# Performance work log

Hardware: AMD Instinct MI355X
Metric: run time of the kernel (lower is better)

The kernel has to match this reference:

```python
import jax, jax.numpy as jnp
import numpy as np


def gru_cell(x, h, Wi, Wh, bi, bh):
    # PyTorch GRU gate order: r, z, n
    gi = x @ Wi + bi
    gh = h @ Wh + bh
    ir, iz, inn = jnp.split(gi, 3, axis=-1)
    hr, hz, hn = jnp.split(gh, 3, axis=-1)
    r = jax.nn.sigmoid(ir + hr)
    z = jax.nn.sigmoid(iz + hz)
    n = jnp.tanh(inn + r * hn)
    return (1.0 - z) * n + z * h


def run_gru_dir(emb, lens, Wi, Wh, bi, bh, reverse):
    # Masked GRU emulating pack_padded_sequence: state holds once t >= len,
    # padded output positions are zero (as pad_packed_sequence produces).
    B, S, _ = emb.shape
    H = Wh.shape[0]
    xs = jnp.swapaxes(emb, 0, 1)  # [S, B, E]
    ts = jnp.arange(S)
    if reverse:
        xs = xs[::-1]
        ts = ts[::-1]
    def step(h, inp):
        x, t = inp
        valid = (t < lens)[:, None]
        h_new = jnp.where(valid, gru_cell(x, h, Wi, Wh, bi, bh), h)
        return h_new, jnp.where(valid, h_new, 0.0)
    hT, outs = jax.lax.scan(step, jnp.zeros((B, H), emb.dtype), (xs, ts))
    if reverse:
        outs = outs[::-1]
    return jnp.swapaxes(outs, 0, 1), hT  # [B,S,H], [B,H]


def seq2seq_forward(src, trg, src_lens, enc_embed, Wi_f, Wh_f, bi_f, bh_f,
                    Wi_b, Wh_b, bi_b, bh_b, W_e2d, b_e2d, dec_embed,
                    Wi_d, Wh_d, bi_d, bh_d, Wq, bq, Wk, bk, Wv, bv,
                    W1, b1, W2, b2):
    lens = jnp.clip(src_lens, 1, None)
    emb = enc_embed[src]  # [B,S,E]; dropout is identity in eval
    out_f, h_f = run_gru_dir(emb, lens, Wi_f, Wh_f, bi_f, bh_f, False)
    out_b, h_b = run_gru_dir(emb, lens, Wi_b, Wh_b, bi_b, bh_b, True)
    word_reps = jnp.concatenate([out_f, out_b], axis=-1)  # [B,S,2H]
    sent_rep = jnp.concatenate([h_f, h_b], axis=-1)       # [B,2H]
    hidden0 = jax.nn.gelu(sent_rep @ W_e2d + b_e2d, approximate=False)
    # k/v projections are loop-invariant -> hoist (same math as per-step)
    K = word_reps @ Wk + bk   # [B,S,kq]
    V = word_reps @ Wv + bv   # [B,S,D]
    scale = 1.0 / np.sqrt(Wq.shape[1]).astype(np.float32)
    def dec_step(h_prev, tok):
        e = dec_embed[tok]  # [B,E]
        h = gru_cell(e, h_prev, Wi_d, Wh_d, bi_d, bh_d)
        q = h @ Wq + bq
        alpha = jax.nn.softmax(jnp.einsum('bk,bsk->bs', q, K) * scale, axis=-1)
        attn = jnp.einsum('bs,bsd->bd', alpha, V)
        hid = h + attn
        out = jax.nn.gelu(hid @ W1 + b1, approximate=False) @ W2 + b2
        return hid, out
    toks = trg[:, :-1].T  # [T-1, B]
    _, outs = jax.lax.scan(dec_step, hidden0, toks)  # [T-1, B, V]
    B = trg.shape[0]
    V = W2.shape[1]
    # outputs[:, 0, :] stays zero as in the original preallocated buffer
    return jnp.concatenate(
        [jnp.zeros((B, 1, V), outs.dtype), jnp.swapaxes(outs, 0, 1)], axis=1)


def setup_inputs() -> dict:
    key = jax.random.key(0)
    ks = iter(jax.random.split(key, 32))
    B, S, T = 32, 64, 64
    SV, TV, E, H, D, KQ = 32000, 32000, 256, 512, 512, 64
    def nrm(shape, fan_in):
        return jax.random.normal(next(ks), shape, jnp.float32) / np.sqrt(fan_in).astype(np.float32)
    return {
        'src': jax.random.randint(next(ks), (B, S), 0, SV),
        'trg': jax.random.randint(next(ks), (B, T), 0, TV),
        'src_lens': jax.random.randint(next(ks), (B,), 1, S + 1),
        'enc_embed': jax.random.normal(next(ks), (SV, E), jnp.float32) * 0.1,
        'Wi_f': nrm((E, 3 * H), E), 'Wh_f': nrm((H, 3 * H), H),
        'bi_f': jnp.zeros((3 * H,), jnp.float32), 'bh_f': jnp.zeros((3 * H,), jnp.float32),
        'Wi_b': nrm((E, 3 * H), E), 'Wh_b': nrm((H, 3 * H), H),
        'bi_b': jnp.zeros((3 * H,), jnp.float32), 'bh_b': jnp.zeros((3 * H,), jnp.float32),
        'W_e2d': nrm((2 * H, D), 2 * H), 'b_e2d': jnp.zeros((D,), jnp.float32),
        'dec_embed': jax.random.normal(next(ks), (TV, E), jnp.float32) * 0.1,
        'Wi_d': nrm((E, 3 * D), E), 'Wh_d': nrm((D, 3 * D), D),
        'bi_d': jnp.zeros((3 * D,), jnp.float32), 'bh_d': jnp.zeros((3 * D,), jnp.float32),
        'Wq': nrm((D, KQ), D), 'bq': jnp.zeros((KQ,), jnp.float32),
        'Wk': nrm((2 * H, KQ), 2 * H), 'bk': jnp.zeros((KQ,), jnp.float32),
        'Wv': nrm((2 * H, D), 2 * H), 'bv': jnp.zeros((D,), jnp.float32),
        'W1': nrm((D, D), D), 'b1': jnp.zeros((D,), jnp.float32),
        'W2': nrm((D, TV), D), 'b2': jnp.zeros((TV,), jnp.float32),
    }


def reference(src, trg, src_lens, enc_embed, Wi_f, Wh_f, bi_f, bh_f,
              Wi_b, Wh_b, bi_b, bh_b, W_e2d, b_e2d, dec_embed,
              Wi_d, Wh_d, bi_d, bh_d, Wq, bq, Wk, bk, Wv, bv,
              W1, b1, W2, b2):
    return seq2seq_forward(src, trg, src_lens, enc_embed, Wi_f, Wh_f, bi_f, bh_f,
                           Wi_b, Wh_b, bi_b, bh_b, W_e2d, b_e2d, dec_embed,
                           Wi_d, Wh_d, bi_d, bh_d, Wq, bq, Wk, bk, Wv, bv,
                           W1, b1, W2, b2)
```

## Files before the change

kernel.cpp:

```cpp
#include <hip/hip_runtime.h>
#include <stdint.h>

typedef unsigned short u16;
typedef short v8s __attribute__((ext_vector_type(8)));
typedef float v4f __attribute__((ext_vector_type(4)));

#define DI static __device__ __forceinline__

DI u16 f2bf(float x){ union{float f; uint32_t u;} c; c.f = x; uint32_t r = c.u + 0x7fffu + ((c.u >> 16) & 1u); return (u16)(r >> 16); }
DI float bf2f(u16 b){ union{float f; uint32_t u;} c; c.u = ((uint32_t)b) << 16; return c.f; }
DI float gelu_f(float x){ return 0.5f * x * (1.0f + erff(x * 0.70710678118654752f)); }
DI float sigm(float x){ return 1.0f / (1.0f + expf(-x)); }

__global__ __launch_bounds__(256) void transpose_split_kernel(
    const float* __restrict__ W, u16* __restrict__ hi, u16* __restrict__ lo, int K, int N)
{
    __shared__ float t[32][33];
    int n0 = blockIdx.x * 32, k0 = blockIdx.y * 32;
    int tx = threadIdx.x & 31, ty = threadIdx.x >> 5;
    #pragma unroll
    for (int i = 0; i < 4; i++) {
        int k = k0 + ty + i * 8, n = n0 + tx;
        float v = (k < K && n < N) ? W[(size_t)k * N + n] : 0.f;
        t[ty + i * 8][tx] = v;
    }
    __syncthreads();
    #pragma unroll
    for (int i = 0; i < 4; i++) {
        int n = n0 + ty + i * 8, k = k0 + tx;
        if (n < N && k < K) {
            float v = t[tx][ty + i * 8];
            u16 h = f2bf(v);
            hi[(size_t)n * K + k] = h;
            lo[(size_t)n * K + k] = f2bf(v - bf2f(h));
        }
    }
}

__global__ __launch_bounds__(256) void gather_init_kernel(
    const int* __restrict__ src, const int* __restrict__ trg,
    const float* __restrict__ enc_embed, const float* __restrict__ dec_embed,
    float* __restrict__ embE, float* __restrict__ embD,
    float* __restrict__ hF0, float* __restrict__ hB0)
{
    int r = blockIdx.x, tx = threadIdx.x;
    if (r < 2048) {
        int idx = src[r];
        embE[(size_t)r * 256 + tx] = enc_embed[(size_t)idx * 256 + tx];
    } else if (r < 4064) {
        int rd = r - 2048;
        int t = rd >> 5, b = rd & 31;
        int tok = trg[b * 64 + t];
        embD[(size_t)rd * 256 + tx] = dec_embed[(size_t)tok * 256 + tx];
    } else {
        int i = (r - 4064) * 256 + tx;
        if (i < 16384) hF0[i] = 0.f; else hB0[i - 16384] = 0.f;
    }
}

__global__ __launch_bounds__(256) void gemm_bf16x3_kernel(
    const float* __restrict__ A, const u16* __restrict__ Bhi, const u16* __restrict__ Blo,
    const float* __restrict__ bias, float* __restrict__ C,
    int M, int N, int K, int act_gelu, int remap)
{
    __shared__ u16 Ah[128 * 40], Al[128 * 40], Bh[128 * 40], Bl[128 * 40];
    const int tid = threadIdx.x;
    const int lane = tid & 63, wave = tid >> 6;
    const int lm = lane & 15, quad = lane >> 4;
    const int wm = wave >> 1, wn = wave & 1;
    const int m0 = blockIdx.y * 128, n0 = blockIdx.x * 128;
    const int sr = tid >> 1;
    const int sh = (tid & 1) * 16;

    v4f acc[4][4];
    #pragma unroll
    for (int i = 0; i < 4; i++)
        #pragma unroll
        for (int j = 0; j < 4; j++)
            #pragma unroll
            for (int r = 0; r < 4; r++) acc[i][j][r] = 0.f;

    for (int k0 = 0; k0 < K; k0 += 32) {
        {
            float v[16];
            const int gm = m0 + sr;
            if (gm < M) {
                const float4* p = (const float4*)(A + (size_t)gm * K + k0 + sh);
                #pragma unroll
                for (int i = 0; i < 4; i++) {
                    float4 q = p[i];
                    v[4*i] = q.x; v[4*i+1] = q.y; v[4*i+2] = q.z; v[4*i+3] = q.w;
                }
            } else {
                #pragma unroll
                for (int i = 0; i < 16; i++) v[i] = 0.f;
            }
            v8s h0, h1, l0, l1;
            #pragma unroll
            for (int i = 0; i < 8; i++) {
                u16 ha = f2bf(v[i]);     u16 la = f2bf(v[i] - bf2f(ha));
                u16 hb = f2bf(v[8+i]);   u16 lb = f2bf(v[8+i] - bf2f(hb));
                h0[i] = (short)ha; l0[i] = (short)la; h1[i] = (short)hb; l1[i] = (short)lb;
            }
            *(v8s*)&Ah[sr * 40 + sh] = h0; *(v8s*)&Ah[sr * 40 + sh + 8] = h1;
            *(v8s*)&Al[sr * 40 + sh] = l0; *(v8s*)&Al[sr * 40 + sh + 8] = l1;
        }
        {
            const int gn = n0 + sr;
            v8s b0, b1, c0, c1;
            if (gn < N) {
                const v8s* ph = (const v8s*)(Bhi + (size_t)gn * K + k0 + sh);
                const v8s* pl = (const v8s*)(Blo + (size_t)gn * K + k0 + sh);
                b0 = ph[0]; b1 = ph[1]; c0 = pl[0]; c1 = pl[1];
            } else {
                #pragma unroll
                for (int i = 0; i < 8; i++) { b0[i] = 0; b1[i] = 0; c0[i] = 0; c1[i] = 0; }
            }
            *(v8s*)&Bh[sr * 40 + sh] = b0; *(v8s*)&Bh[sr * 40 + sh + 8] = b1;
            *(v8s*)&Bl[sr * 40 + sh] = c0; *(v8s*)&Bl[sr * 40 + sh + 8] = c1;
        }
        __syncthreads();
        v8s ah[4], al[4], bh[4], bl[4];
        #pragma unroll
        for (int mt = 0; mt < 4; mt++) {
            int off = (wm * 64 + mt * 16 + lm) * 40 + quad * 8;
            ah[mt] = *(v8s*)&Ah[off]; al[mt] = *(v8s*)&Al[off];
        }
        #pragma unroll
        for (int nt = 0; nt < 4; nt++) {
            int off = (wn * 64 + nt * 16 + lm) * 40 + quad * 8;
            bh[nt] = *(v8s*)&Bh[off]; bl[nt] = *(v8s*)&Bl[off];
        }
        #pragma unroll
        for (int mt = 0; mt < 4; mt++)
            #pragma unroll
            for (int nt = 0; nt < 4; nt++) {
                v4f a = acc[mt][nt];
                a = __builtin_amdgcn_mfma_f32_16x16x32_bf16(ah[mt], bh[nt], a, 0, 0, 0);
                a = __builtin_amdgcn_mfma_f32_16x16x32_bf16(ah[mt], bl[nt], a, 0, 0, 0);
                a = __builtin_amdgcn_mfma_f32_16x16x32_bf16(al[mt], bh[nt], a, 0, 0, 0);
                acc[mt][nt] = a;
            }
        __syncthreads();
    }
    #pragma unroll
    for (int nt = 0; nt < 4; nt++) {
        int col = n0 + wn * 64 + nt * 16 + lm;
        if (col >= N) continue;
        float bv = bias ? bias[col] : 0.f;
        #pragma unroll
        for (int mt = 0; mt < 4; mt++) {
            int rbase = m0 + wm * 64 + mt * 16 + quad * 4;
            #pragma unroll
            for (int r = 0; r < 4; r++) {
                int row = rbase + r;
                if (row < M) {
                    float v = acc[mt][nt][r] + bv;
                    if (act_gelu) v = gelu_f(v);
                    size_t drow = remap ? (size_t)((row & 31) * 64 + (row >> 5) + 1) : (size_t)row;
                    C[drow * (size_t)N + col] = v;
                }
            }
        }
    }
}

DI float gru_out(float i0, float i1, float i2, float g0, float g1, float g2,
                 float b0, float b1, float b2, float hprev)
{
    float r = sigm(i0 + g0 + b0);
    float z = sigm(i1 + g1 + b1);
    float n = tanhf(i2 + r * (g2 + b2));
    return (1.f - z) * n + z * hprev;
}

__global__ __launch_bounds__(256) void enc_step_kernel(
    int step,
    const float* __restrict__ hFin, float* __restrict__ hFout,
    const float* __restrict__ hBin, float* __restrict__ hBout,
    const float* __restrict__ giF, const float* __restrict__ giB,
    const float* __restrict__ Wh_f, const float* __restrict__ Wh_b,
    const float* __restrict__ bh_f, const float* __restrict__ bh_b,
    const int* __restrict__ src_lens,
    float* __restrict__ wrep, float* __restrict__ sent)
{
    const int dir = blockIdx.x >> 6;
    const int jb = (blockIdx.x & 63) * 8;
    const int tid = threadIdx.x;
    const int b = tid >> 3, jj = tid & 7, j = jb + jj;
    const float* hin = dir ? hBin : hFin;
    const float* gi  = dir ? giB : giF;
    const float* Wh  = dir ? Wh_b : Wh_f;
    const float* bh  = dir ? bh_b : bh_f;
    float* hout = dir ? hBout : hFout;
    const int t_eff = dir ? (63 - step) : step;

    __shared__ float hl[32 * 132];
    float g0 = 0.f, g1 = 0.f, g2 = 0.f;
    for (int kt = 0; kt < 512; kt += 128) {
        __syncthreads();
        #pragma unroll
        for (int w = 0; w < 4; w++) {
            int flat = (tid + w * 256) * 4;
            int bb = flat >> 7, kk = flat & 127;
            float4 fv = *(const float4*)(hin + bb * 512 + kt + kk);
            *(float4*)&hl[bb * 132 + kk] = fv;
        }
        __syncthreads();
        const float* w0base = Wh + (size_t)kt * 1536 + j;
        #pragma unroll 2
        for (int kk = 0; kk < 128; kk += 4) {
            float4 hv = *(const float4*)&hl[b * 132 + kk];
            const float* w = w0base + (size_t)kk * 1536;
            g0 += hv.x * w[0];    g1 += hv.x * w[512];  g2 += hv.x * w[1024];
            g0 += hv.y * w[1536]; g1 += hv.y * w[2048]; g2 += hv.y * w[2560];
            g0 += hv.z * w[3072]; g1 += hv.z * w[3584]; g2 += hv.z * w[4096];
            g0 += hv.w * w[4608]; g1 += hv.w * w[5120]; g2 += hv.w * w[5632];
        }
    }
    size_t gbase = ((size_t)b * 64 + t_eff) * 1536 + j;
    float hprev = hin[b * 512 + j];
    float hnew = gru_out(gi[gbase], gi[gbase + 512], gi[gbase + 1024],
                         g0, g1, g2, bh[j], bh[512 + j], bh[1024 + j], hprev);
    int len = src_lens[b]; if (len < 1) len = 1;
    bool valid = t_eff < len;
    float hkeep = valid ? hnew : hprev;
    hout[b * 512 + j] = hkeep;
    wrep[((size_t)b * 64 + t_eff) * 1024 + dir * 512 + j] = valid ? hnew : 0.f;
    if (step == 63) sent[b * 1024 + dir * 512 + j] = hkeep;
}

__global__ __launch_bounds__(256) void dec_cell_kernel(
    int t, const float* __restrict__ HID, const float* __restrict__ giD,
    const float* __restrict__ Wh, const float* __restrict__ bh,
    float* __restrict__ htmp)
{
    const int jb = blockIdx.x * 8;
    const int tid = threadIdx.x;
    const int b = tid >> 3, jj = tid & 7, j = jb + jj;
    const float* hin = HID + (size_t)t * 16384;

    __shared__ float hl[32 * 132];
    float g0 = 0.f, g1 = 0.f, g2 = 0.f;
    for (int kt = 0; kt < 512; kt += 128) {
        __syncthreads();
        #pragma unroll
        for (int w = 0; w < 4; w++) {
            int flat = (tid + w * 256) * 4;
            int bb = flat >> 7, kk = flat & 127;
            float4 fv = *(const float4*)(hin + bb * 512 + kt + kk);
            *(float4*)&hl[bb * 132 + kk] = fv;
        }
        __syncthreads();
        const float* w0base = Wh + (size_t)kt * 1536 + j;
        #pragma unroll 2
        for (int kk = 0; kk < 128; kk += 4) {
            float4 hv = *(const float4*)&hl[b * 132 + kk];
            const float* w = w0base + (size_t)kk * 1536;
            g0 += hv.x * w[0];    g1 += hv.x * w[512];  g2 += hv.x * w[1024];
            g0 += hv.y * w[1536]; g1 += hv.y * w[2048]; g2 += hv.y * w[2560];
            g0 += hv.z * w[3072]; g1 += hv.z * w[3584]; g2 += hv.z * w[4096];
            g0 += hv.w * w[4608]; g1 += hv.w * w[5120]; g2 += hv.w * w[5632];
        }
    }
    size_t gbase = ((size_t)t * 32 + b) * 1536 + j;
    float hprev = hin[b * 512 + j];
    float hnew = gru_out(giD[gbase], giD[gbase + 512], giD[gbase + 1024],
                         g0, g1, g2, bh[j], bh[512 + j], bh[1024 + j], hprev);
    htmp[b * 512 + j] = hnew;
}

__global__ __launch_bounds__(256) void dec_attn_kernel(
    int t, const float* __restrict__ htmp, const float* __restrict__ Kmat,
    const float* __restrict__ Vmat, const float* __restrict__ Wq,
    const float* __restrict__ bq, float* __restrict__ HID)
{
    const int b = blockIdx.x, tid = threadIdx.x;
    __shared__ float hl[512];
    __shared__ float Kt[64 * 68];
    __shared__ float qp[256];
    __shared__ float qv[64];
    __shared__ float aw[64];

    hl[tid] = htmp[b * 512 + tid];
    hl[256 + tid] = htmp[b * 512 + 256 + tid];
    #pragma unroll
    for (int w = 0; w < 4; w++) {
        int flat = (tid + w * 256) * 4;
        int s = flat >> 6, d = flat & 63;
        float4 fv = *(const float4*)(Kmat + ((size_t)b * 64 + s) * 64 + d);
        *(float4*)&Kt[s * 68 + d] = fv;
    }
    __syncthreads();
    {
        int o = tid >> 2, part = tid & 3;
        float acc = 0.f;
        const float* wq = Wq + (size_t)(part * 128) * 64 + o;
        int base = part * 128;
        for (int k = 0; k < 128; k++) acc += hl[base + k] * wq[(size_t)k * 64];
        qp[tid] = acc;
    }
    __syncthreads();
    if (tid < 64) qv[tid] = qp[tid * 4] + qp[tid * 4 + 1] + qp[tid * 4 + 2] + qp[tid * 4 + 3] + bq[tid];
    __syncthreads();
    if (tid < 64) {
        float sc = 0.f;
        #pragma unroll 8
        for (int d = 0; d < 64; d++) sc += qv[d] * Kt[tid * 68 + d];
        sc *= 0.125f;
        float mx = sc;
        #pragma unroll
        for (int m = 32; m >= 1; m >>= 1) mx = fmaxf(mx, __shfl_xor(mx, m));
        float e = expf(sc - mx);
        float sm = e;
        #pragma unroll
        for (int m = 32; m >= 1; m >>= 1) sm += __shfl_xor(sm, m);
        aw[tid] = e / sm;
    }
    __syncthreads();
    float* hid = HID + ((size_t)(t + 1)) * 16384 + (size_t)b * 512;
    #pragma unroll
    for (int c = 0; c < 2; c++) {
        int jcol = tid + c * 256;
        float acc = 0.f;
        for (int s = 0; s < 64; s++) acc += aw[s] * Vmat[((size_t)b * 64 + s) * 512 + jcol];
        hid[jcol] = hl[jcol] + acc;
    }
}

__global__ __launch_bounds__(256) void zero_col0_kernel(float* __restrict__ out)
{
    int gid = blockIdx.x * 256 + threadIdx.x;
    if (gid < 32 * 32000) {
        int b = gid / 32000, col = gid % 32000;
        out[(size_t)b * 64 * 32000 + col] = 0.f;
    }
}

extern "C" void kernel_launch(void* const* d_in, const int* in_sizes, int n_in,
                              void* d_out, int out_size, void* d_ws, size_t ws_size,
                              hipStream_t stream)
{
    const int*   src       = (const int*)d_in[0];
    const int*   trg       = (const int*)d_in[1];
    const int*   src_lens  = (const int*)d_in[2];
    const float* enc_embed = (const float*)d_in[3];
    const float* Wi_f  = (const float*)d_in[4];
    const float* Wh_f  = (const float*)d_in[5];
    const float* bi_f  = (const float*)d_in[6];
    const float* bh_f  = (const float*)d_in[7];
    const float* Wi_b  = (const float*)d_in[8];
    const float* Wh_b  = (const float*)d_in[9];
    const float* bi_b  = (const float*)d_in[10];
    const float* bh_b  = (const float*)d_in[11];
    const float* W_e2d = (const float*)d_in[12];
    const float* b_e2d = (const float*)d_in[13];
    const float* dec_embed = (const float*)d_in[14];
    const float* Wi_d  = (const float*)d_in[15];
    const float* Wh_d  = (const float*)d_in[16];
    const float* bi_d  = (const float*)d_in[17];
    const float* bh_d  = (const float*)d_in[18];
    const float* Wq    = (const float*)d_in[19];
    const float* bq    = (const float*)d_in[20];
    const float* Wk    = (const float*)d_in[21];
    const float* bk    = (const float*)d_in[22];
    const float* Wv    = (const float*)d_in[23];
    const float* bv    = (const float*)d_in[24];
    const float* W1    = (const float*)d_in[25];
    const float* b1    = (const float*)d_in[26];
    const float* W2    = (const float*)d_in[27];
    const float* b2    = (const float*)d_in[28];
    float* out = (float*)d_out;

    float* f = (float*)d_ws;
    float* embE = f; f += 524288;
    float* embD = f; f += 516096;
    float* giF  = f; f += 3145728;
    float* giB  = f; f += 3145728;
    float* giD  = f; f += 3096576;
    float* wrep = f; f += 2097152;
    float* sent = f; f += 32768;
    float* hF   = f; f += 32768;
    float* hB   = f; f += 32768;
    float* Kmat = f; f += 131072;
    float* Vmat = f; f += 1048576;
    float* HID  = f; f += 1048576;
    float* htmp = f; f += 16384;
    float* G1   = f; f += 1032192;
    u16* u = (u16*)f;
    u16* WiF_hi = u; u += 393216;  u16* WiF_lo = u; u += 393216;
    u16* WiB_hi = u; u += 393216;  u16* WiB_lo = u; u += 393216;
    u16* WiD_hi = u; u += 393216;  u16* WiD_lo = u; u += 393216;
    u16* Wk_hi  = u; u += 65536;   u16* Wk_lo  = u; u += 65536;
    u16* Wv_hi  = u; u += 524288;  u16* Wv_lo  = u; u += 524288;
    u16* We_hi  = u; u += 524288;  u16* We_lo  = u; u += 524288;
    u16* W1_hi  = u; u += 262144;  u16* W1_lo  = u; u += 262144;
    u16* W2_hi  = u; u += 16384000; u16* W2_lo = u; u += 16384000;

    hipLaunchKernelGGL(transpose_split_kernel, dim3(48, 8),   dim3(256), 0, stream, Wi_f,  WiF_hi, WiF_lo, 256, 1536);
    hipLaunchKernelGGL(transpose_split_kernel, dim3(48, 8),   dim3(256), 0, stream, Wi_b,  WiB_hi, WiB_lo, 256, 1536);
    hipLaunchKernelGGL(transpose_split_kernel, dim3(48, 8),   dim3(256), 0, stream, Wi_d,  WiD_hi, WiD_lo, 256, 1536);
    hipLaunchKernelGGL(transpose_split_kernel, dim3(2, 32),   dim3(256), 0, stream, Wk,    Wk_hi,  Wk_lo,  1024, 64);
    hipLaunchKernelGGL(transpose_split_kernel, dim3(16, 32),  dim3(256), 0, stream, Wv,    Wv_hi,  Wv_lo,  1024, 512);
    hipLaunchKernelGGL(transpose_split_kernel, dim3(16, 32),  dim3(256), 0, stream, W_e2d, We_hi,  We_lo,  1024, 512);
    hipLaunchKernelGGL(transpose_split_kernel, dim3(16, 16),  dim3(256), 0, stream, W1,    W1_hi,  W1_lo,  512, 512);
    hipLaunchKernelGGL(transpose_split_kernel, dim3(1000, 16),dim3(256), 0, stream, W2,    W2_hi,  W2_lo,  512, 32000);

    hipLaunchKernelGGL(gather_init_kernel, dim3(4192), dim3(256), 0, stream,
                       src, trg, enc_embed, dec_embed, embE, embD, hF, hB);

    hipLaunchKernelGGL(gemm_bf16x3_kernel, dim3(12, 16), dim3(256), 0, stream,
                       embE, WiF_hi, WiF_lo, bi_f, giF, 2048, 1536, 256, 0, 0);
    hipLaunchKernelGGL(gemm_bf16x3_kernel, dim3(12, 16), dim3(256), 0, stream,
                       embE, WiB_hi, WiB_lo, bi_b, giB, 2048, 1536, 256, 0, 0);
    hipLaunchKernelGGL(gemm_bf16x3_kernel, dim3(12, 16), dim3(256), 0, stream,
                       embD, WiD_hi, WiD_lo, bi_d, giD, 2016, 1536, 256, 0, 0);

    for (int step = 0; step < 64; step++) {
        const float* hFin = hF + (step & 1) * 16384;
        float*       hFout = hF + ((step + 1) & 1) * 16384;
        const float* hBin = hB + (step & 1) * 16384;
        float*       hBout = hB + ((step + 1) & 1) * 16384;
        hipLaunchKernelGGL(enc_step_kernel, dim3(128), dim3(256), 0, stream,
                           step, hFin, hFout, hBin, hBout, giF, giB,
                           Wh_f, Wh_b, bh_f, bh_b, src_lens, wrep, sent);
    }

    hipLaunchKernelGGL(gemm_bf16x3_kernel, dim3(1, 16), dim3(256), 0, stream,
                       wrep, Wk_hi, Wk_lo, bk, Kmat, 2048, 64, 1024, 0, 0);
    hipLaunchKernelGGL(gemm_bf16x3_kernel, dim3(4, 16), dim3(256), 0, stream,
                       wrep, Wv_hi, Wv_lo, bv, Vmat, 2048, 512, 1024, 0, 0);
    hipLaunchKernelGGL(gemm_bf16x3_kernel, dim3(4, 1), dim3(256), 0, stream,
                       sent, We_hi, We_lo, b_e2d, HID, 32, 512, 1024, 1, 0);

    for (int t = 0; t < 63; t++) {
        hipLaunchKernelGGL(dec_cell_kernel, dim3(64), dim3(256), 0, stream,
                           t, HID, giD, Wh_d, bh_d, htmp);
        hipLaunchKernelGGL(dec_attn_kernel, dim3(32), dim3(256), 0, stream,
                           t, htmp, Kmat, Vmat, Wq, bq, HID);
    }

    hipLaunchKernelGGL(gemm_bf16x3_kernel, dim3(4, 16), dim3(256), 0, stream,
                       HID + 16384, W1_hi, W1_lo, b1, G1, 2016, 512, 512, 1, 0);
    hipLaunchKernelGGL(gemm_bf16x3_kernel, dim3(250, 16), dim3(256), 0, stream,
                       G1, W2_hi, W2_lo, b2, out, 2016, 32000, 512, 0, 1);

    hipLaunchKernelGGL(zero_col0_kernel, dim3(4000), dim3(256), 0, stream, out);
}
```

Measured before the change: 4.250 ms.

## Replace per-step GRU launches with persistent kernels using grid barriers and LDS-resident weights

Result: slower. 6.933 ms (+63.1%).

```diff
diff --git a/kernel.cpp b/kernel.cpp
--- a/kernel.cpp
+++ b/kernel.cpp
@@ -11,6 +11,28 @@
 DI float bf2f(u16 b){ union{float f; uint32_t u;} c; c.u = ((uint32_t)b) << 16; return c.f; }
 DI float gelu_f(float x){ return 0.5f * x * (1.0f + erff(x * 0.70710678118654752f)); }
 DI float sigm(float x){ return 1.0f / (1.0f + expf(-x)); }
+
+DI float gru_out(float i0, float i1, float i2, float g0, float g1, float g2,
+                 float b0, float b1, float b2, float hprev)
+{
+    float r = sigm(i0 + g0 + b0);
+    float z = sigm(i1 + g1 + b1);
+    float n = tanhf(i2 + r * (g2 + b2));
+    return (1.f - z) * n + z * hprev;
+}
+
+DI void grid_barrier(unsigned* cnt, int id, unsigned nblocks)
+{
+    __syncthreads();
+    if (threadIdx.x == 0) {
+        __threadfence();
+        __hip_atomic_fetch_add(&cnt[id], 1u, __ATOMIC_RELEASE, __HIP_MEMORY_SCOPE_AGENT);
+        while (__hip_atomic_load(&cnt[id], __ATOMIC_ACQUIRE, __HIP_MEMORY_SCOPE_AGENT) < nblocks) {
+            __builtin_amdgcn_s_sleep(1);
+        }
+    }
+    __syncthreads();
+}
 
 __global__ __launch_bounds__(256) void transpose_split_kernel(
     const float* __restrict__ W, u16* __restrict__ hi, u16* __restrict__ lo, int K, int N)
@@ -37,11 +59,30 @@
     }
 }
 
+__global__ __launch_bounds__(256) void transpose_f32_kernel(
+    const float* __restrict__ W, float* __restrict__ WT, int K, int N)
+{
+    __shared__ float t[32][33];
+    int n0 = blockIdx.x * 32, k0 = blockIdx.y * 32;
+    int tx = threadIdx.x & 31, ty = threadIdx.x >> 5;
+    #pragma unroll
+    for (int i = 0; i < 4; i++) {
+        int k = k0 + ty + i * 8, n = n0 + tx;
+        t[ty + i * 8][tx] = (k < K && n < N) ? W[(size_t)k * N + n] : 0.f;
+    }
+    __syncthreads();
+    #pragma unroll
+    for (int i = 0; i < 4; i++) {
+        int n = n0 + ty + i * 8, k = k0 + tx;
+        if (n < N && k < K) WT[(size_t)n * K + k] = t[tx][ty + i * 8];
+    }
+}
+
 __global__ __launch_bounds__(256) void gather_init_kernel(
     const int* __restrict__ src, const int* __restrict__ trg,
     const float* __restrict__ enc_embed, const float* __restrict__ dec_embed,
     float* __restrict__ embE, float* __restrict__ embD,
-    float* __restrict__ hF0, float* __restrict__ hB0)
+    float* __restrict__ hF0, float* __restrict__ hB0, unsigned* __restrict__ bar)
 {
     int r = blockIdx.x, tx = threadIdx.x;
     if (r < 2048) {
@@ -52,9 +93,11 @@
         int t = rd >> 5, b = rd & 31;
         int tok = trg[b * 64 + t];
         embD[(size_t)rd * 256 + tx] = dec_embed[(size_t)tok * 256 + tx];
-    } else {
+    } else if (r < 4192) {
         int i = (r - 4064) * 256 + tx;
         if (i < 16384) hF0[i] = 0.f; else hB0[i - 16384] = 0.f;
+    } else {
+        bar[tx] = 0u;
     }
 }
 
@@ -68,7 +111,9 @@
     const int lane = tid & 63, wave = tid >> 6;
     const int lm = lane & 15, quad = lane >> 4;
     const int wm = wave >> 1, wn = wave & 1;
-    const int m0 = blockIdx.y * 128, n0 = blockIdx.x * 128;
+    const int bid = blockIdx.y * gridDim.x + blockIdx.x;
+    const int mt = bid % gridDim.y, nt_ = bid / gridDim.y;
+    const int m0 = mt * 128, n0 = nt_ * 128;
     const int sr = tid >> 1;
     const int sh = (tid & 1) * 16;
 
@@ -122,40 +167,40 @@
         __syncthreads();
         v8s ah[4], al[4], bh[4], bl[4];
         #pragma unroll
-        for (int mt = 0; mt < 4; mt++) {
-            int off = (wm * 64 + mt * 16 + lm) * 40 + quad * 8;
-            ah[mt] = *(v8s*)&Ah[off]; al[mt] = *(v8s*)&Al[off];
-        }
-        #pragma unroll
-        for (int nt = 0; nt < 4; nt++) {
-            int off = (wn * 64 + nt * 16 + lm) * 40 + quad * 8;
-            bh[nt] = *(v8s*)&Bh[off]; bl[nt] = *(v8s*)&Bl[off];
-        }
-        #pragma unroll
-        for (int mt = 0; mt < 4; mt++)
-            #pragma unroll
-            for (int nt = 0; nt < 4; nt++) {
-                v4f a = acc[mt][nt];
-                a = __builtin_amdgcn_mfma_f32_16x16x32_bf16(ah[mt], bh[nt], a, 0, 0, 0);
-                a = __builtin_amdgcn_mfma_f32_16x16x32_bf16(ah[mt], bl[nt], a, 0, 0, 0);
-                a = __builtin_amdgcn_mfma_f32_16x16x32_bf16(al[mt], bh[nt], a, 0, 0, 0);
-                acc[mt][nt] = a;
+        for (int mt2 = 0; mt2 < 4; mt2++) {
+            int off = (wm * 64 + mt2 * 16 + lm) * 40 + quad * 8;
+            ah[mt2] = *(v8s*)&Ah[off]; al[mt2] = *(v8s*)&Al[off];
+        }
+        #pragma unroll
+        for (int nt2 = 0; nt2 < 4; nt2++) {
+            int off = (wn * 64 + nt2 * 16 + lm) * 40 + quad * 8;
+            bh[nt2] = *(v8s*)&Bh[off]; bl[nt2] = *(v8s*)&Bl[off];
+        }
+        #pragma unroll
+        for (int mt2 = 0; mt2 < 4; mt2++)
+            #pragma unroll
+            for (int nt2 = 0; nt2 < 4; nt2++) {
+                v4f a = acc[mt2][nt2];
+                a = __builtin_amdgcn_mfma_f32_16x16x32_bf16(ah[mt2], bh[nt2], a, 0, 0, 0);
+                a = __builtin_amdgcn_mfma_f32_16x16x32_bf16(ah[mt2], bl[nt2], a, 0, 0, 0);
+                a = __builtin_amdgcn_mfma_f32_16x16x32_bf16(al[mt2], bh[nt2], a, 0, 0, 0);
+                acc[mt2][nt2] = a;
             }
         __syncthreads();
     }
     #pragma unroll
-    for (int nt = 0; nt < 4; nt++) {
-        int col = n0 + wn * 64 + nt * 16 + lm;
+    for (int nt2 = 0; nt2 < 4; nt2++) {
+        int col = n0 + wn * 64 + nt2 * 16 + lm;
         if (col >= N) continue;
         float bv = bias ? bias[col] : 0.f;
         #pragma unroll
-        for (int mt = 0; mt < 4; mt++) {
-            int rbase = m0 + wm * 64 + mt * 16 + quad * 4;
+        for (int mt2 = 0; mt2 < 4; mt2++) {
+            int rbase = m0 + wm * 64 + mt2 * 16 + quad * 4;
             #pragma unroll
             for (int r = 0; r < 4; r++) {
                 int row = rbase + r;
                 if (row < M) {
-                    float v = acc[mt][nt][r] + bv;
+                    float v = acc[mt2][nt2][r] + bv;
                     if (act_gelu) v = gelu_f(v);
                     size_t drow = remap ? (size_t)((row & 31) * 64 + (row >> 5) + 1) : (size_t)row;
                     C[drow * (size_t)N + col] = v;
@@ -165,166 +210,221 @@
     }
 }
 
-DI float gru_out(float i0, float i1, float i2, float g0, float g1, float g2,
-                 float b0, float b1, float b2, float hprev)
-{
-    float r = sigm(i0 + g0 + b0);
-    float z = sigm(i1 + g1 + b1);
-    float n = tanhf(i2 + r * (g2 + b2));
-    return (1.f - z) * n + z * hprev;
-}
-
-__global__ __launch_bounds__(256) void enc_step_kernel(
-    int step,
-    const float* __restrict__ hFin, float* __restrict__ hFout,
-    const float* __restrict__ hBin, float* __restrict__ hBout,
+DI void recur_mm(const float* __restrict__ hin, const float* __restrict__ wl,
+                 float* __restrict__ hl, int tid, int jj, int kseg, int bq,
+                 float acc[3][4])
+{
+    #pragma unroll
+    for (int half = 0; half < 2; half++) {
+        __syncthreads();
+        #pragma unroll
+        for (int it = 0; it < 8; it++) {
+            int q = tid + it * 256;
+            int b = q >> 6, kl = (q & 63) * 4;
+            float4 v = *(const float4*)(hin + b * 512 + half * 256 + kl);
+            *(float4*)&hl[b * 292 + (kl >> 5) * 36 + (kl & 31)] = v;
+        }
+        __syncthreads();
+        const int wko = (half * 4 + (kseg >> 1)) * 72 + (kseg & 1) * 36;
+        const float* w0 = &wl[jj * 580 + wko];
+        const float* w1 = &wl[(4 + jj) * 580 + wko];
+        const float* w2 = &wl[(8 + jj) * 580 + wko];
+        const float* h0 = &hl[(bq * 4) * 292 + kseg * 36];
+        const float* h1 = h0 + 292;
+        const float* h2 = h1 + 292;
+        const float* h3 = h2 + 292;
+        #pragma unroll
+        for (int kk = 0; kk < 32; kk += 4) {
+            float4 a0 = *(const float4*)(w0 + kk);
+            float4 a1 = *(const float4*)(w1 + kk);
+            float4 a2 = *(const float4*)(w2 + kk);
+            float4 hv0 = *(const float4*)(h0 + kk);
+            float4 hv1 = *(const float4*)(h1 + kk);
+            float4 hv2 = *(const float4*)(h2 + kk);
+            float4 hv3 = *(const float4*)(h3 + kk);
+#define ACC4(g, i, av, hv) acc[g][i] = fmaf(hv.w, av.w, fmaf(hv.z, av.z, fmaf(hv.y, av.y, fmaf(hv.x, av.x, acc[g][i]))))
+            ACC4(0,0,a0,hv0); ACC4(1,0,a1,hv0); ACC4(2,0,a2,hv0);
+            ACC4(0,1,a0,hv1); ACC4(1,1,a1,hv1); ACC4(2,1,a2,hv1);
+            ACC4(0,2,a0,hv2); ACC4(1,2,a1,hv2); ACC4(2,2,a2,hv2);
+            ACC4(0,3,a0,hv3); ACC4(1,3,a1,hv3); ACC4(2,3,a2,hv3);
+#undef ACC4
+        }
+    }
+}
+
+DI void load_weights_lds(const float* __restrict__ WhT, int jb, int tid, float* __restrict__ wl)
+{
+    for (int q = tid; q < 12 * 128; q += 256) {
+        int c = q >> 7;
+        int k4 = (q & 127) * 4;
+        int gate = c >> 2, j4 = c & 3;
+        float4 w = *(const float4*)(WhT + ((size_t)(gate * 512 + jb + j4)) * 512 + k4);
+        *(float4*)&wl[c * 580 + (k4 >> 6) * 72 + ((k4 >> 5) & 1) * 36 + (k4 & 31)] = w;
+    }
+}
+
+__global__ __launch_bounds__(256, 1) void enc_persistent_kernel(
+    const float* __restrict__ WhT_f, const float* __restrict__ WhT_b,
+    const float* __restrict__ bh_f, const float* __restrict__ bh_b,
     const float* __restrict__ giF, const float* __restrict__ giB,
-    const float* __restrict__ Wh_f, const float* __restrict__ Wh_b,
-    const float* __restrict__ bh_f, const float* __restrict__ bh_b,
     const int* __restrict__ src_lens,
-    float* __restrict__ wrep, float* __restrict__ sent)
-{
-    const int dir = blockIdx.x >> 6;
-    const int jb = (blockIdx.x & 63) * 8;
+    float* __restrict__ hF, float* __restrict__ hB,
+    float* __restrict__ wrep, float* __restrict__ sent, unsigned* __restrict__ bar)
+{
+    __shared__ float wl[6960];
+    __shared__ float hl[9344];
     const int tid = threadIdx.x;
-    const int b = tid >> 3, jj = tid & 7, j = jb + jj;
-    const float* hin = dir ? hBin : hFin;
+    const int dir = blockIdx.x >> 7;
+    const int jb = (blockIdx.x & 127) * 4;
+    const int bq = tid >> 5, jj = (tid >> 3) & 3, kseg = tid & 7;
+    const int j = jb + jj;
+    const float* WhT = dir ? WhT_b : WhT_f;
     const float* gi  = dir ? giB : giF;
-    const float* Wh  = dir ? Wh_b : Wh_f;
-    const float* bh  = dir ? bh_b : bh_f;
-    float* hout = dir ? hBout : hFout;
-    const int t_eff = dir ? (63 - step) : step;
-
-    __shared__ float hl[32 * 132];
-    float g0 = 0.f, g1 = 0.f, g2 = 0.f;
-    for (int kt = 0; kt < 512; kt += 128) {
-        __syncthreads();
-        #pragma unroll
-        for (int w = 0; w < 4; w++) {
-            int flat = (tid + w * 256) * 4;
-            int bb = flat >> 7, kk = flat & 127;
-            float4 fv = *(const float4*)(hin + bb * 512 + kt + kk);
-            *(float4*)&hl[bb * 132 + kk] = fv;
-        }
-        __syncthreads();
-        const float* w0base = Wh + (size_t)kt * 1536 + j;
-        #pragma unroll 2
-        for (int kk = 0; kk < 128; kk += 4) {
-            float4 hv = *(const float4*)&hl[b * 132 + kk];
-            const float* w = w0base + (size_t)kk * 1536;
-            g0 += hv.x * w[0];    g1 += hv.x * w[512];  g2 += hv.x * w[1024];
-            g0 += hv.y * w[1536]; g1 += hv.y * w[2048]; g2 += hv.y * w[2560];
-            g0 += hv.z * w[3072]; g1 += hv.z * w[3584]; g2 += hv.z * w[4096];
-            g0 += hv.w * w[4608]; g1 += hv.w * w[5120]; g2 += hv.w * w[5632];
-        }
-    }
-    size_t gbase = ((size_t)b * 64 + t_eff) * 1536 + j;
-    float hprev = hin[b * 512 + j];
-    float hnew = gru_out(gi[gbase], gi[gbase + 512], gi[gbase + 1024],
-                         g0, g1, g2, bh[j], bh[512 + j], bh[1024 + j], hprev);
-    int len = src_lens[b]; if (len < 1) len = 1;
-    bool valid = t_eff < len;
-    float hkeep = valid ? hnew : hprev;
-    hout[b * 512 + j] = hkeep;
-    wrep[((size_t)b * 64 + t_eff) * 1024 + dir * 512 + j] = valid ? hnew : 0.f;
-    if (step == 63) sent[b * 1024 + dir * 512 + j] = hkeep;
-}
-
-__global__ __launch_bounds__(256) void dec_cell_kernel(
-    int t, const float* __restrict__ HID, const float* __restrict__ giD,
-    const float* __restrict__ Wh, const float* __restrict__ bh,
-    float* __restrict__ htmp)
-{
-    const int jb = blockIdx.x * 8;
+    const float* bhp = dir ? bh_b : bh_f;
+    float* hping = dir ? hB : hF;
+
+    load_weights_lds(WhT, jb, tid, wl);
+    float bh0 = 0.f, bh1 = 0.f, bh2 = 0.f;
+    int len[4] = {1,1,1,1};
+    if (kseg == 0) {
+        bh0 = bhp[j]; bh1 = bhp[512 + j]; bh2 = bhp[1024 + j];
+        #pragma unroll
+        for (int i = 0; i < 4; i++) { int l = src_lens[bq * 4 + i]; len[i] = l < 1 ? 1 : l; }
+    }
+
+    for (int step = 0; step < 64; step++) {
+        const float* hin = hping + (step & 1) * 16384;
+        float* hout = hping + ((step + 1) & 1) * 16384;
+        float acc[3][4] = {};
+        recur_mm(hin, wl, hl, tid, jj, kseg, bq, acc);
+        #pragma unroll
+        for (int g = 0; g < 3; g++)
+            #pragma unroll
+            for (int i = 0; i < 4; i++) {
+                float v = acc[g][i];
+                v += __shfl_xor(v, 1); v += __shfl_xor(v, 2); v += __shfl_xor(v, 4);
+                acc[g][i] = v;
+            }
+        const int t_eff = dir ? (63 - step) : step;
+        if (kseg == 0) {
+            #pragma unroll
+            for (int i = 0; i < 4; i++) {
+                int b = bq * 4 + i;
+                size_t gb = ((size_t)b * 64 + t_eff) * 1536 + j;
+                float hprev = hin[b * 512 + j];
+                float hnew = gru_out(gi[gb], gi[gb + 512], gi[gb + 1024],
+                                     acc[0][i], acc[1][i], acc[2][i],
+                                     bh0, bh1, bh2, hprev);
+                bool valid = t_eff < len[i];
+                float hkeep = valid ? hnew : hprev;
+                hout[b * 512 + j] = hkeep;
+                wrep[((size_t)b * 64 + t_eff) * 1024 + dir * 512 + j] = valid ? hnew : 0.f;
+                if (step == 63) sent[b * 1024 + dir * 512 + j] = hkeep;
+            }
+        }
+        grid_barrier(bar, step, 256u);
+    }
+}
+
+__global__ __launch_bounds__(256, 1) void dec_persistent_kernel(
+    const float* __restrict__ WhT_d, const float* __restrict__ bh_d,
+    const float* __restrict__ giD,
+    const float* __restrict__ Kmat, const float* __restrict__ Vmat,
+    const float* __restrict__ Wq, const float* __restrict__ bqv,
+    float* __restrict__ HID, float* __restrict__ htmp, unsigned* __restrict__ bar)
+{
+    __shared__ float wl[6960];
+    __shared__ float hl[9344];
     const int tid = threadIdx.x;
-    const int b = tid >> 3, jj = tid & 7, j = jb + jj;
-    const float* hin = HID + (size_t)t * 16384;
-
-    __shared__ float hl[32 * 132];
-    float g0 = 0.f, g1 = 0.f, g2 = 0.f;
-    for (int kt = 0; kt < 512; kt += 128) {
-        __syncthreads();
-        #pragma unroll
-        for (int w = 0; w < 4; w++) {
-            int flat = (tid + w * 256) * 4;
-            int bb = flat >> 7, kk = flat & 127;
-            float4 fv = *(const float4*)(hin + bb * 512 + kt + kk);
-            *(float4*)&hl[bb * 132 + kk] = fv;
-        }
-        __syncthreads();
-        const float* w0base = Wh + (size_t)kt * 1536 + j;
-        #pragma unroll 2
-        for (int kk = 0; kk < 128; kk += 4) {
-            float4 hv = *(const float4*)&hl[b * 132 + kk];
-            const float* w = w0base + (size_t)kk * 1536;
-            g0 += hv.x * w[0];    g1 += hv.x * w[512];  g2 += hv.x * w[1024];
-            g0 += hv.y * w[1536]; g1 += hv.y * w[2048]; g2 += hv.y * w[2560];
-            g0 += hv.z * w[3072]; g1 += hv.z * w[3584]; g2 += hv.z * w[4096];
-            g0 += hv.w * w[4608]; g1 += hv.w * w[5120]; g2 += hv.w * w[5632];
-        }
-    }
-    size_t gbase = ((size_t)t * 32 + b) * 1536 + j;
-    float hprev = hin[b * 512 + j];
-    float hnew = gru_out(giD[gbase], giD[gbase + 512], giD[gbase + 1024],
-                         g0, g1, g2, bh[j], bh[512 + j], bh[1024 + j], hprev);
-    htmp[b * 512 + j] = hnew;
-}
-
-__global__ __launch_bounds__(256) void dec_attn_kernel(
-    int t, const float* __restrict__ htmp, const float* __restrict__ Kmat,
-    const float* __restrict__ Vmat, const float* __restrict__ Wq,
-    const float* __restrict__ bq, float* __restrict__ HID)
-{
-    const int b = blockIdx.x, tid = threadIdx.x;
-    __shared__ float hl[512];
-    __shared__ float Kt[64 * 68];
-    __shared__ float qp[256];
-    __shared__ float qv[64];
-    __shared__ float aw[64];
-
-    hl[tid] = htmp[b * 512 + tid];
-    hl[256 + tid] = htmp[b * 512 + 256 + tid];
-    #pragma unroll
-    for (int w = 0; w < 4; w++) {
-        int flat = (tid + w * 256) * 4;
-        int s = flat >> 6, d = flat & 63;
-        float4 fv = *(const float4*)(Kmat + ((size_t)b * 64 + s) * 64 + d);
-        *(float4*)&Kt[s * 68 + d] = fv;
-    }
-    __syncthreads();
-    {
-        int o = tid >> 2, part = tid & 3;
-        float acc = 0.f;
-        const float* wq = Wq + (size_t)(part * 128) * 64 + o;
-        int base = part * 128;
-        for (int k = 0; k < 128; k++) acc += hl[base + k] * wq[(size_t)k * 64];
-        qp[tid] = acc;
-    }
-    __syncthreads();
-    if (tid < 64) qv[tid] = qp[tid * 4] + qp[tid * 4 + 1] + qp[tid * 4 + 2] + qp[tid * 4 + 3] + bq[tid];
-    __syncthreads();
-    if (tid < 64) {
-        float sc = 0.f;
-        #pragma unroll 8
-        for (int d = 0; d < 64; d++) sc += qv[d] * Kt[tid * 68 + d];
-        sc *= 0.125f;
-        float mx = sc;
-        #pragma unroll
-        for (int m = 32; m >= 1; m >>= 1) mx = fmaxf(mx, __shfl_xor(mx, m));
-        float e = expf(sc - mx);
-        float sm = e;
-        #pragma unroll
-        for (int m = 32; m >= 1; m >>= 1) sm += __shfl_xor(sm, m);
-        aw[tid] = e / sm;
-    }
-    __syncthreads();
-    float* hid = HID + ((size_t)(t + 1)) * 16384 + (size_t)b * 512;
-    #pragma unroll
-    for (int c = 0; c < 2; c++) {
-        int jcol = tid + c * 256;
-        float acc = 0.f;
-        for (int s = 0; s < 64; s++) acc += aw[s] * Vmat[((size_t)b * 64 + s) * 512 + jcol];
-        hid[jcol] = hl[jcol] + acc;
+    const int jb = blockIdx.x * 4;
+    const int bq = tid >> 5, jj = (tid >> 3) & 3, kseg = tid & 7;
+    const int j = jb + jj;
+
+    load_weights_lds(WhT_d, jb, tid, wl);
+    float bh0 = 0.f, bh1 = 0.f, bh2 = 0.f;
+    if (kseg == 0) { bh0 = bh_d[j]; bh1 = bh_d[512 + j]; bh2 = bh_d[1024 + j]; }
+
+    for (int t = 0; t < 63; t++) {
+        const float* hin = HID + (size_t)t * 16384;
+        float acc[3][4] = {};
+        recur_mm(hin, wl, hl, tid, jj, kseg, bq, acc);
+        #pragma unroll
+        for (int g = 0; g < 3; g++)
+            #pragma unroll
+            for (int i = 0; i < 4; i++) {
+                float v = acc[g][i];
+                v += __shfl_xor(v, 1); v += __shfl_xor(v, 2); v += __shfl_xor(v, 4);
+                acc[g][i] = v;
+            }
+        if (kseg == 0) {
+            #pragma unroll
+            for (int i = 0; i < 4; i++) {
+                int b = bq * 4 + i;
+                size_t gb = ((size_t)t * 32 + b) * 1536 + j;
+                float hprev = hin[b * 512 + j];
+                float hnew = gru_out(giD[gb], giD[gb + 512], giD[gb + 1024],
+                                     acc[0][i], acc[1][i], acc[2][i],
+                                     bh0, bh1, bh2, hprev);
+                htmp[b * 512 + j] = hnew;
+            }
+        }
+        grid_barrier(bar, 2 * t, 128u);
+
+        if (blockIdx.x < 32) {
+            const int b = blockIdx.x;
+            float* Kt  = hl;
+            float* hl2 = hl + 4352;
+            float* qv  = hl + 4864;
+            float* aw  = hl + 4928;
+            #pragma unroll
+            for (int it = 0; it < 4; it++) {
+                int q = tid + it * 256;
+                int s = q >> 4, d = (q & 15) * 4;
+                float4 v = *(const float4*)(Kmat + ((size_t)b * 64 + s) * 64 + d);
+                *(float4*)&Kt[s * 68 + d] = v;
+            }
+            if (tid < 128) {
+                float4 v = *(const float4*)(htmp + b * 512 + tid * 4);
+                *(float4*)&hl2[tid * 4] = v;
+            }
+            __syncthreads();
+            {
+                int o = tid >> 2, part = tid & 3;
+                float a = 0.f;
+                const float* wqp = Wq + (size_t)(part * 128) * 64 + o;
+                const float* hp = hl2 + part * 128;
+                #pragma unroll 4
+                for (int k = 0; k < 128; k++) a = fmaf(hp[k], wqp[(size_t)k * 64], a);
+                a += __shfl_xor(a, 1); a += __shfl_xor(a, 2);
+                if (part == 0) qv[o] = a + bqv[o];
+            }
+            __syncthreads();
+            if (tid < 64) {
+                float sc = 0.f;
+                #pragma unroll 8
+                for (int d = 0; d < 64; d++) sc = fmaf(qv[d], Kt[tid * 68 + d], sc);
+                sc *= 0.125f;
+                float mx = sc;
+                #pragma unroll
+                for (int m = 32; m >= 1; m >>= 1) mx = fmaxf(mx, __shfl_xor(mx, m));
+                float e = expf(sc - mx);
+                float sm = e;
+                #pragma unroll
+                for (int m = 32; m >= 1; m >>= 1) sm += __shfl_xor(sm, m);
+                aw[tid] = e / sm;
+            }
+            __syncthreads();
+            float* hid = HID + (size_t)(t + 1) * 16384 + (size_t)b * 512;
+            #pragma unroll
+            for (int c = 0; c < 2; c++) {
+                int col = tid + c * 256;
+                float a = 0.f;
+                #pragma unroll 4
+                for (int s = 0; s < 64; s++) a = fmaf(aw[s], Vmat[((size_t)b * 64 + s) * 512 + col], a);
+                hid[col] = hl2[col] + a;
+            }
+        }
+        grid_barrier(bar, 2 * t + 1, 128u);
     }
 }
 
@@ -387,6 +487,10 @@
     float* HID  = f; f += 1048576;
     float* htmp = f; f += 16384;
     float* G1   = f; f += 1032192;
+    float* WhTf = f; f += 786432;
+    float* WhTb = f; f += 786432;
+    float* WhTd = f; f += 786432;
+    unsigned* bar = (unsigned*)f; f += 256;
     u16* u = (u16*)f;
     u16* WiF_hi = u; u += 393216;  u16* WiF_lo = u; u += 393216;
     u16* WiB_hi = u; u += 393216;  u16* WiB_lo = u; u += 393216;
@@ -405,9 +509,12 @@
     hipLaunchKernelGGL(transpose_split_kernel, dim3(16, 32),  dim3(256), 0, stream, W_e2d, We_hi,  We_lo,  1024, 512);
     hipLaunchKernelGGL(transpose_split_kernel, dim3(16, 16),  dim3(256), 0, stream, W1,    W1_hi,  W1_lo,  512, 512);
     hipLaunchKernelGGL(transpose_split_kernel, dim3(1000, 16),dim3(256), 0, stream, W2,    W2_hi,  W2_lo,  512, 32000);
-
-    hipLaunchKernelGGL(gather_init_kernel, dim3(4192), dim3(256), 0, stream,
-                       src, trg, enc_embed, dec_embed, embE, embD, hF, hB);
+    hipLaunchKernelGGL(transpose_f32_kernel,   dim3(48, 16),  dim3(256), 0, stream, Wh_f,  WhTf, 512, 1536);
+    hipLaunchKernelGGL(transpose_f32_kernel,   dim3(48, 16),  dim3(256), 0, stream, Wh_b,  WhTb, 512, 1536);
+    hipLaunchKernelGGL(transpose_f32_kernel,   dim3(48, 16),  dim3(256), 0, stream, Wh_d,  WhTd, 512, 1536);
+
+    hipLaunchKernelGGL(gather_init_kernel, dim3(4193), dim3(256), 0, stream,
+                       src, trg, enc_embed, dec_embed, embE, embD, hF, hB, bar);
 
     hipLaunchKernelGGL(gemm_bf16x3_kernel, dim3(12, 16), dim3(256), 0, stream,
                        embE, WiF_hi, WiF_lo, bi_f, giF, 2048, 1536, 256, 0, 0);
@@ -416,15 +523,9 @@
     hipLaunchKernelGGL(gemm_bf16x3_kernel, dim3(12, 16), dim3(256), 0, stream,
                        embD, WiD_hi, WiD_lo, bi_d, giD, 2016, 1536, 256, 0, 0);
 
-    for (int step = 0; step < 64; step++) {
-        const float* hFin = hF + (step & 1) * 16384;
-        float*       hFout = hF + ((step + 1) & 1) * 16384;
-        const float* hBin = hB + (step & 1) * 16384;
-        float*       hBout = hB + ((step + 1) & 1) * 16384;
-        hipLaunchKernelGGL(enc_step_kernel, dim3(128), dim3(256), 0, stream,
-                           step, hFin, hFout, hBin, hBout, giF, giB,
-                           Wh_f, Wh_b, bh_f, bh_b, src_lens, wrep, sent);
-    }
+    hipLaunchKernelGGL(enc_persistent_kernel, dim3(256), dim3(256), 0, stream,
+                       WhTf, WhTb, bh_f, bh_b, giF, giB, src_lens,
+                       hF, hB, wrep, sent, bar);
 
     hipLaunchKernelGGL(gemm_bf16x3_kernel, dim3(1, 16), dim3(256), 0, stream,
                        wrep, Wk_hi, Wk_lo, bk, Kmat, 2048, 64, 1024, 0, 0);
@@ -433,12 +534,8 @@
     hipLaunchKernelGGL(gemm_bf16x3_kernel, dim3(4, 1), dim3(256), 0, stream,
                        sent, We_hi, We_lo, b_e2d, HID, 32, 512, 1024, 1, 0);
 
-    for (int t = 0; t < 63; t++) {
-        hipLaunchKernelGGL(dec_cell_kernel, dim3(64), dim3(256), 0, stream,
-                           t, HID, giD, Wh_d, bh_d, htmp);
-        hipLaunchKernelGGL(dec_attn_kernel, dim3(32), dim3(256), 0, stream,
-                           t, htmp, Kmat, Vmat, Wq, bq, HID);
-    }
+    hipLaunchKernelGGL(dec_persistent_kernel, dim3(128), dim3(256), 0, stream,
+                       WhTd, bh_d, giD, Kmat, Vmat, Wq, bq, HID, htmp, bar + 64);
 
     hipLaunchKernelGGL(gemm_bf16x3_kernel, dim3(4, 16), dim3(256), 0, stream,
                        HID + 16384, W1_hi, W1_lo, b1, G1, 2016, 512, 512, 1, 0);
```
